# Kernel optimization log

Hardware: AMD Instinct MI355X
Metric: run time of the kernel (lower is better)

The kernel has to match this reference:

```python
import jax, jax.numpy as jnp
import numpy as np
from jax import lax

ANCHOR_LENGTHS = (1.0, 2.0, 3.0, 4.0, 5.0, 7.0, 9.0)
B, C, LF = 8, 512, 8192
A = len(ANCHOR_LENGTHS)
PRE_K, POST_K = 600, 100          # pre/post NMS topk (propose defaults)
SCORE_TH, IOU_TH = 0.1, 0.5


def setup_inputs() -> dict:
    key = jax.random.key(0)
    ks = jax.random.split(key, 7)
    def n(k, shape, scale=1.0):
        return jax.random.normal(k, shape, dtype=jnp.float32) * scale
    return {
        "feat": n(ks[0], (B, C, LF)),
        "conv_w": n(ks[1], (C, C, 3), 0.02),
        "conv_b": n(ks[2], (C,), 0.02),
        "obj_w": n(ks[3], (A, C), 0.02),
        "obj_b": n(ks[4], (A,), 0.02),
        "reg_w": n(ks[5], (2 * A, C), 0.02),
        "reg_b": n(ks[6], (2 * A,), 0.02),
    }


def make_anchors_1d(Lf):
    lengths = jnp.asarray(ANCHOR_LENGTHS, jnp.float32)  # [A]
    centers = jnp.arange(Lf, dtype=jnp.float32) + 0.5   # [Lf]
    start = centers[:, None] - 0.5 * lengths[None, :]
    end = centers[:, None] + 0.5 * lengths[None, :]
    return jnp.stack([start, end], axis=-1).reshape(Lf * A, 2)  # [Lf*A, 2]


def decode_deltas_to_boxes(anchors, deltas, Lf):
    # anchors [N,2], deltas [B,N,2]
    a_c = 0.5 * (anchors[:, 0] + anchors[:, 1])
    a_w = jnp.clip(anchors[:, 1] - anchors[:, 0], 1e-6)
    t_c = deltas[..., 0]
    t_w = jnp.clip(deltas[..., 1], -10.0, 10.0)
    c = a_c[None, :] + t_c * a_w[None, :]
    w = a_w[None, :] * jnp.exp(t_w)
    Lff = jnp.float32(Lf)
    start = jnp.clip(c - 0.5 * w, 0.0, Lff)
    end = jnp.clip(c + 0.5 * w, 0.0, Lff)
    eps = 1e-3
    end = jnp.minimum(jnp.maximum(end, start + eps), Lff)
    start = jnp.maximum(jnp.minimum(start, end - eps), 0.0)
    return jnp.stack([start, end], axis=-1)  # [B,N,2]


def _nms_keep(boxes, valid):
    # boxes [K,2] already sorted by descending score; valid [K] bool
    s, e = boxes[:, 0], boxes[:, 1]
    inter = jnp.clip(jnp.minimum(e[:, None], e[None, :]) -
                     jnp.maximum(s[:, None], s[None, :]), 0.0)
    w = e - s
    union = w[:, None] + w[None, :] - inter
    iou = inter / jnp.clip(union, 1e-6)  # [K,K]; matches torchvision 2D trick (y-extent 1)
    idx = jnp.arange(boxes.shape[0])
    def body(i, keep):
        sup = jnp.any(keep & (idx < i) & (iou[i] > IOU_TH))
        return keep.at[i].set(keep[i] & jnp.logical_not(sup))
    return lax.fori_loop(0, boxes.shape[0], body, valid)


def propose(obj_logits, boxes):
    # fixed-shape, batched version of RPN1D.propose (no fallback path):
    # outputs are padded to POST_K with a validity mask.
    scores = jax.nn.sigmoid(obj_logits)                    # [B,N]
    s_top, idx = lax.top_k(scores, PRE_K)                  # sorted desc
    bxs = jnp.take_along_axis(boxes, idx[:, :, None], axis=1)  # [B,K,2]
    valid = s_top >= SCORE_TH
    keep = jax.vmap(_nms_keep)(bxs, valid)                 # [B,K]
    s_kept = jnp.where(keep, s_top, -1.0)
    s_out, j = lax.top_k(s_kept, POST_K)                   # kept, in score order
    b_out = jnp.take_along_axis(bxs, j[:, :, None], axis=1)
    vmask = s_out > 0.0
    return (jnp.where(vmask[:, :, None], b_out, 0.0),
            jnp.where(vmask, s_out, 0.0),
            vmask)


def reference(feat, conv_w, conv_b, obj_w, obj_b, reg_w, reg_b):
    # feat [B,C,Lf]; conv1d k=3 pad=1 + relu
    h = lax.conv_general_dilated(feat, conv_w, window_strides=(1,),
                                 padding=((1, 1),),
                                 dimension_numbers=("NCH", "OIH", "NCH"))
    h = jax.nn.relu(h + conv_b[None, :, None])
    x = jnp.transpose(h, (0, 2, 1))                        # [B,Lf,C]
    obj = jnp.einsum("blc,ac->bla", x, obj_w) + obj_b      # [B,Lf,A]
    reg = jnp.einsum("blc,ac->bla", x, reg_w) + reg_b      # [B,Lf,2A]
    Bsz, Lf = x.shape[0], x.shape[1]
    obj = obj.reshape(Bsz, Lf * A)                          # [B,N]
    reg = reg.reshape(Bsz, Lf * A, 2)                       # [B,N,2]
    anchors = make_anchors_1d(Lf)                           # [N,2]
    boxes = decode_deltas_to_boxes(anchors, reg, Lf)        # [B,N,2]
    props, pscores, pmask = propose(obj, boxes)
    return obj, reg, anchors, props, pscores, pmask
```

## Files before the change

kernel.cpp:

```cpp
#include <hip/hip_runtime.h>

#define LF 8192
#define NB 8
#define NC 512
#define NA 7
#define NANCH 57344
#define PRE_K 600
#define POST_K 100

#define OBJ_OFF   0
#define REG_OFF   458752
#define ANCH_OFF  1376256
#define PROPS_OFF 1490944
#define PSC_OFF   1492544
#define PM_OFF    1493344

#define WF_BYTES   3145728
#define GHIST_OFF  WF_BYTES
#define GHIST_BYTES (8 * 65536 * 4)

typedef __attribute__((ext_vector_type(8))) short bf16x8;
typedef __attribute__((ext_vector_type(4))) float f32x4;

__device__ __forceinline__ unsigned short f2bf(float f) {
  unsigned u = __float_as_uint(f);
  u += 0x7fff + ((u >> 16) & 1);
  return (unsigned short)(u >> 16);
}
__device__ __forceinline__ float bf2f(unsigned short h) {
  return __uint_as_float(((unsigned)h) << 16);
}

__device__ __forceinline__ void cvt_split(float v0, float v1,
                                          unsigned& hw, unsigned& lw) {
  asm("v_cvt_pk_bf16_f32 %0, %1, %2" : "=v"(hw) : "v"(v0), "v"(v1));
  float h0f = __uint_as_float(hw << 16);
  float h1f = __uint_as_float(hw & 0xffff0000u);
  asm("v_cvt_pk_bf16_f32 %0, %1, %2" : "=v"(lw) : "v"(v0 - h0f), "v"(v1 - h1f));
}

__global__ void prep_w_k(const float* __restrict__ cw, unsigned short* __restrict__ wf,
                         float* __restrict__ out, unsigned* __restrict__ ghist) {
  int o = blockIdx.x * 256 + threadIdx.x;
  {
    size_t z = 2 * (size_t)o;
    if (z < ANCH_OFF) {
      out[z] = 0.f;
      if (z + 1 < ANCH_OFF) out[z + 1] = 0.f;
    }
  }
  if (o < 8 * 65536) ghist[o] = 0u;
  if (o < NANCH) {
    int l = o / 7, a = o - l * 7;
    float len = (float)(a + 1 + (a > 4 ? a - 4 : 0));
    float c = (float)l + 0.5f;
    out[ANCH_OFF + 2 * (size_t)o]     = c - 0.5f * len;
    out[ANCH_OFF + 2 * (size_t)o + 1] = c + 0.5f * len;
  }
  if (o >= 786432) return;
  int j    = o & 7;
  int lane = (o >> 3) & 63;
  int cotl = (o >> 9) & 7;
  int rem  = o >> 12;
  int tap  = rem % 3;
  int cc   = rem / 3;
  int co = (cc >> 4) * 128 + cotl * 16 + (lane & 15);
  int ci = (cc & 15) * 32 + (lane >> 4) * 8 + j;
  float w = cw[((size_t)co * 512 + ci) * 3 + tap];
  unsigned short hi = f2bf(w);
  unsigned short lo = f2bf(w - bf2f(hi));
  size_t base = ((((size_t)rem * 8 + cotl) * 2) * 64 + lane) * 8 + j;
  wf[base] = hi;
  wf[base + 512] = lo;
}

#define BUFSH 10400
__global__ __launch_bounds__(256) void conv_proj_k(
    const float* __restrict__ feat, const unsigned short* __restrict__ wfrag,
    const float* __restrict__ cbias, const float* __restrict__ obj_w,
    const float* __restrict__ obj_b, const float* __restrict__ reg_w,
    const float* __restrict__ reg_b, float* __restrict__ out)
{
  __shared__ __align__(16) char smem[41600];
  unsigned short* sb = (unsigned short*)smem;
  float* bufp = (float*)smem;

  const int tid  = threadIdx.x;
  const int l0   = blockIdx.x * 128;
  const int cob  = blockIdx.y;
  const int b    = blockIdx.z;
  const int lane = tid & 63, wave = tid >> 6;
  const int wm = wave >> 1, wn = wave & 1;
  const int quad = lane >> 4, l15 = lane & 15;

  const float* fb = feat + (size_t)b * 512 * LF;
  const bf16x8* wf8 = (const bf16x8*)wfrag;

  f32x4 acc[4][4];
  #pragma unroll
  for (int mt = 0; mt < 4; ++mt)
    #pragma unroll
    for (int nt = 0; nt < 4; ++nt) acc[mt][nt] = (f32x4){0.f, 0.f, 0.f, 0.f};

  const int r8 = tid & 7, cp2 = (tid >> 3) & 15, set = tid >> 7;

  const int brr = tid >> 4, bc2 = tid & 15;
  const int bl = (brr == 0) ? (l0 - 1) : (l0 + 128);
  const bool bok = (bl >= 0) && (bl < LF);

  float pv0[8], pv1[8], bv0 = 0.f, bv1 = 0.f;

  auto prefetch = [&](int ch) {
    const int cb = ch * 32;
    #pragma unroll
    for (int p = 0; p < 8; ++p) {
      int l = l0 + p * 16 + set * 8 + r8;
      pv0[p] = fb[(size_t)(cb + 2 * cp2) * LF + l];
      pv1[p] = fb[(size_t)(cb + 2 * cp2 + 1) * LF + l];
    }
    if (tid < 32 && bok) {
      bv0 = fb[(size_t)(cb + 2 * bc2) * LF + bl];
      bv1 = fb[(size_t)(cb + 2 * bc2 + 1) * LF + bl];
    }
  };
  auto stage = [&](int bi) {
    unsigned short* fh = sb + bi * BUFSH;
    unsigned short* fl = fh + 5200;
    #pragma unroll
    for (int p = 0; p < 8; ++p) {
      int row = p * 16 + set * 8 + r8;
      unsigned hw, lw;
      cvt_split(pv0[p], pv1[p], hw, lw);
      int e = (row + 1) * 40 + 2 * cp2;
      *(unsigned*)(fh + e) = hw;
      *(unsigned*)(fl + e) = lw;
    }
    if (tid < 32) {
      unsigned hw, lw;
      cvt_split(bv0, bv1, hw, lw);
      int e = (brr * 129) * 40 + 2 * bc2;
      *(unsigned*)(fh + e) = hw;
      *(unsigned*)(fl + e) = lw;
    }
  };

  prefetch(0);
  stage(0);
  prefetch(1);
  __syncthreads();

  for (int chunk = 0; chunk < 16; ++chunk) {
    const unsigned short* fh = sb + (chunk & 1) * BUFSH;
    const unsigned short* fl = fh + 5200;
    const int rem3 = (cob * 16 + chunk) * 3;

    bf16x8 AhA[4], AlA[4], AhB[4], AlB[4];
    bf16x8 Bh[4], Bl[4];

    auto loadA = [&](int tap, bf16x8* AH, bf16x8* AL) {
      #pragma unroll
      for (int mt = 0; mt < 4; ++mt) {
        int fi = (((rem3 + tap) * 8 + wm * 4 + mt) * 2) * 64 + lane;
        AH[mt] = wf8[fi];
        AL[mt] = wf8[fi + 64];
      }
    };
    auto loadB = [&](int tap) {
      #pragma unroll
      for (int nt = 0; nt < 4; ++nt) {
        int row = wn * 64 + nt * 16 + l15 + tap;
        int e = row * 40 + quad * 8;
        Bh[nt] = *(const bf16x8*)(fh + e);
        Bl[nt] = *(const bf16x8*)(fl + e);
      }
    };
    auto mfma_tap = [&](const bf16x8* AH, const bf16x8* AL) {
      __builtin_amdgcn_s_setprio(1);
      #pragma unroll
      for (int mt = 0; mt < 4; ++mt)
        #pragma unroll
        for (int nt = 0; nt < 4; ++nt) {
          acc[mt][nt] = __builtin_amdgcn_mfma_f32_16x16x32_bf16(AH[mt], Bh[nt], acc[mt][nt], 0, 0, 0);
          acc[mt][nt] = __builtin_amdgcn_mfma_f32_16x16x32_bf16(AH[mt], Bl[nt], acc[mt][nt], 0, 0, 0);
          acc[mt][nt] = __builtin_amdgcn_mfma_f32_16x16x32_bf16(AL[mt], Bh[nt], acc[mt][nt], 0, 0, 0);
        }
      __builtin_amdgcn_s_setprio(0);
    };

    loadA(0, AhA, AlA);
    if (chunk < 15) stage((chunk + 1) & 1);
    loadB(0);
    loadA(1, AhB, AlB);
    __builtin_amdgcn_sched_barrier(0);
    mfma_tap(AhA, AlA);
    loadB(1);
    loadA(2, AhA, AlA);
    __builtin_amdgcn_sched_barrier(0);
    mfma_tap(AhB, AlB);
    loadB(2);
    if (chunk < 14) prefetch(chunk + 2);
    mfma_tap(AhA, AlA);
    __syncthreads();
  }

  const int sg = tid >> 5;
  const int ll = tid & 31;
  int rc0 = 3 * sg     < 21 ? 3 * sg     : 20;
  int rc1 = 3 * sg + 1 < 21 ? 3 * sg + 1 : 20;
  int rc2 = 3 * sg + 2 < 21 ? 3 * sg + 2 : 20;
  const float* wr0 = (rc0 < 7) ? (obj_w + (size_t)rc0 * 512) : (reg_w + (size_t)(rc0 - 7) * 512);
  const float* wr1 = (rc1 < 7) ? (obj_w + (size_t)rc1 * 512) : (reg_w + (size_t)(rc1 - 7) * 512);
  const float* wr2 = (rc2 < 7) ? (obj_w + (size_t)rc2 * 512) : (reg_w + (size_t)(rc2 - 7) * 512);
  float pacc[3][4];
  #pragma unroll
  for (int q = 0; q < 3; ++q)
    #pragma unroll
    for (int m = 0; m < 4; ++m) pacc[q][m] = 0.f;

  #pragma unroll
  for (int h = 0; h < 2; ++h) {
    __syncthreads();
    if (wm == h) {
      #pragma unroll
      for (int mt = 0; mt < 4; ++mt) {
        f32x4 bv = *(const f32x4*)(cbias + cob * 128 + h * 64 + mt * 16 + quad * 4);
        #pragma unroll
        for (int nt = 0; nt < 4; ++nt) {
          int col = wn * 64 + nt * 16 + l15;
          #pragma unroll
          for (int r = 0; r < 4; ++r)
            bufp[(mt * 16 + quad * 4 + r) * 130 + col] = fmaxf(acc[mt][nt][r] + bv[r], 0.f);
        }
      }
    }
    __syncthreads();
    for (int c = 0; c < 64; ++c) {
      int cg = cob * 128 + h * 64 + c;
      float w0 = wr0[cg], w1 = wr1[cg], w2 = wr2[cg];
      #pragma unroll
      for (int m = 0; m < 4; ++m) {
        float hv = bufp[c * 130 + ll + 32 * m];
        pacc[0][m] = fmaf(w0, hv, pacc[0][m]);
        pacc[1][m] = fmaf(w1, hv, pacc[1][m]);
        pacc[2][m] = fmaf(w2, hv, pacc[2][m]);
      }
    }
  }

  const size_t ob = (size_t)b * NANCH;
  #pragma unroll
  for (int q = 0; q < 3; ++q) {
    int r = 3 * sg + q;
    if (r < 21) {
      #pragma unroll
      for (int m = 0; m < 4; ++m) {
        int l = l0 + ll + 32 * m;
        float v = pacc[q][m] + ((cob == 0) ? ((r < 7) ? obj_b[r] : reg_b[r - 7]) : 0.f);
        if (r < 7) atomicAdd(&out[OBJ_OFF + ob + (size_t)l * 7 + r], v);
        else { int rr = r - 7; atomicAdd(&out[REG_OFF + (ob + (size_t)l * 7 + (rr >> 1)) * 2 + (rr & 1)], v); }
      }
    }
  }
}

__device__ __forceinline__ unsigned keybits(float x) {
  unsigned u = __float_as_uint(x);
  return (u & 0x80000000u) ? ~u : (u | 0x80000000u);
}

__global__ __launch_bounds__(256) void hist_k(const float* __restrict__ out,
                                              unsigned* __restrict__ ghist) {
  const int b = blockIdx.y;
  const float* obj = out + OBJ_OFF + (size_t)b * NANCH;
  unsigned* h = ghist + (size_t)b * 65536;
  const int base = blockIdx.x * 256 + threadIdx.x;
  float v[8];
  #pragma unroll
  for (int k = 0; k < 8; ++k) v[k] = obj[base + k * 7168];
  #pragma unroll
  for (int k = 0; k < 8; ++k) {
    unsigned bin = keybits(v[k]) >> 16;
    unsigned phys = ((bin & 255u) << 8) | (bin >> 8);
    atomicAdd(&h[phys], 1u);
  }
}

__global__ __launch_bounds__(1024) void propose_k(float* __restrict__ out,
                                                  const unsigned* __restrict__ ghist) {
  const int b = blockIdx.x;
  const int tid = threadIdx.x;
  const int lane = tid & 63;
  const int wave = tid >> 6;

  __shared__ unsigned long long pool[PRE_K * 10];
  __shared__ unsigned part[1024];
  __shared__ unsigned coarse[256];
  __shared__ float bs[PRE_K], be[PRE_K], bsc[PRE_K];
  __shared__ unsigned long long vwords[10];
  __shared__ int scal[6];

  unsigned long long* keys = pool;
  const float* obj = out + OBJ_OFF + (size_t)b * NANCH;
  const unsigned* gh = ghist + (size_t)b * 65536;

  if (tid < 10) vwords[tid] = 0ull;
  if (tid == 0) scal[2] = 0;

  {
    const int q = tid >> 8, h8 = tid & 255;
    unsigned s = 0;
    #pragma unroll 8
    for (int lo = 0; lo < 64; ++lo) s += gh[((unsigned)(q * 64 + lo) << 8) | (unsigned)h8];
    part[tid] = s;
  }
  __syncthreads();
  if (tid < 256) coarse[tid] = part[tid] + part[tid + 256] + part[tid + 512] + part[tid + 768];
  __syncthreads();
  for (int off = 1; off < 256; off <<= 1) {
    unsigned v = 0, add = 0;
    if (tid < 256) { v = coarse[tid]; add = (tid + off < 256) ? coarse[tid + off] : 0u; }
    __syncthreads();
    if (tid < 256) coarse[tid] = v + add;
    __syncthreads();
  }
  if (tid < 256) {
    unsigned sfx  = coarse[tid];
    unsigned sfx1 = (tid < 255) ? coarse[tid + 1] : 0u;
    if (sfx >= (unsigned)PRE_K && sfx1 < (unsigned)PRE_K) { scal[0] = tid; scal[1] = (int)sfx1; }
  }
  __syncthreads();
  const int hi8 = scal[0];
  const int before1 = scal[1];
  __syncthreads();
  if (tid < 256) coarse[tid] = gh[((unsigned)tid << 8) | (unsigned)hi8];
  __syncthreads();
  for (int off = 1; off < 256; off <<= 1) {
    unsigned v = 0, add = 0;
    if (tid < 256) { v = coarse[tid]; add = (tid + off < 256) ? coarse[tid + off] : 0u; }
    __syncthreads();
    if (tid < 256) coarse[tid] = v + add;
    __syncthreads();
  }
  if (tid < 256) {
    unsigned sfx  = coarse[tid];
    unsigned sfx1 = (tid < 255) ? coarse[tid + 1] : 0u;
    if (before1 + (int)sfx >= PRE_K && before1 + (int)sfx1 < PRE_K) scal[4] = tid;
  }
  __syncthreads();
  const unsigned Tbits = ((((unsigned)hi8 << 8) | (unsigned)scal[4]) << 16);

  for (int it = 0; it < 7; ++it) {
    float v[8];
    #pragma unroll
    for (int k = 0; k < 8; ++k) v[k] = obj[it * 8192 + k * 1024 + tid];
    #pragma unroll
    for (int k = 0; k < 8; ++k) {
      unsigned u = keybits(v[k]);
      if (u >= Tbits) {
        int p = atomicAdd(&scal[2], 1);
        if (p < 1024)
          keys[p] = ((unsigned long long)u << 32) |
                    (unsigned long long)(~(unsigned)(it * 8192 + k * 1024 + tid));
      }
    }
  }
  __syncthreads();
  const int cnt = scal[2];
  if (tid >= cnt) keys[tid] = 0ull;
  for (unsigned k = 2; k <= 1024; k <<= 1) {
    for (unsigned j = k >> 1; j > 0; j >>= 1) {
      __syncthreads();
      unsigned idx = tid, partner = idx ^ j;
      if (partner > idx) {
        unsigned long long a = keys[idx], c = keys[partner];
        bool up = ((idx & k) == 0);
        if (up ? (a < c) : (a > c)) { keys[idx] = c; keys[partner] = a; }
      }
    }
  }
  __syncthreads();
  if (tid < PRE_K) {
    const int t = tid;
    unsigned long long kv = keys[t];
    unsigned u  = (unsigned)(kv >> 32);
    unsigned i2 = ~((unsigned)kv);
    unsigned ub = (u & 0x80000000u) ? (u & 0x7fffffffu) : ~u;
    float logit = __uint_as_float(ub);
    float score = 1.f / (1.f + expf(-logit));
    int li = (int)(i2 / 7u);
    int a  = (int)(i2 - (unsigned)li * 7u);
    float alen = (float)(a + 1 + (a > 4 ? a - 4 : 0));
    const float* rp = out + REG_OFF + ((size_t)b * NANCH + i2) * 2;
    float tc = rp[0];
    float tw = fminf(fmaxf(rp[1], -10.f), 10.f);
    float cc = (float)li + 0.5f + tc * alen;
    float ww = alen * expf(tw);
    float s0 = cc - 0.5f * ww;
    float e0 = cc + 0.5f * ww;
    s0 = fminf(fmaxf(s0, 0.f), (float)LF);
    e0 = fminf(fmaxf(e0, 0.f), (float)LF);
    e0 = fminf(fmaxf(e0, s0 + 1e-3f), (float)LF);
    s0 = fmaxf(fminf(s0, e0 - 1e-3f), 0.f);
    bs[t] = s0; be[t] = e0; bsc[t] = score;
    if (score >= 0.1f) atomicOr(&vwords[t >> 6], 1ull << (t & 63));
  }
  __syncthreads();
  for (int widx = tid; widx < PRE_K * 10; widx += 1024) {
    int j = widx / 10;
    int w = widx - j * 10;
    int base = w * 64;
    unsigned long long m = 0ull;
    if (base + 63 > j) {
      float sj = bs[j], ej = be[j];
      float wj = ej - sj;
      for (int bit = 0; bit < 64; ++bit) {
        int i3 = base + bit;
        if (i3 > j && i3 < PRE_K) {
          float inter = fmaxf(fminf(ej, be[i3]) - fmaxf(sj, bs[i3]), 0.f);
          float uni = wj + (be[i3] - bs[i3]) - inter;
          float iou = inter / fmaxf(uni, 1e-6f);
          if (iou > 0.5f) m |= (1ull << bit);
        }
      }
    }
    pool[widx] = m;
  }
  __syncthreads();
  if (wave == 0) {
    unsigned long long rem = 0ull;
    unsigned long long vw = (lane < 10) ? vwords[lane] : 0ull;
    unsigned long long mrow = (lane < 10) ? pool[lane] : 0ull;
    int kept = 0;
    for (int g = 0; g < PRE_K && kept < POST_K; g += 8) {
      unsigned long long n0 = (lane < 10 && g + 1 < PRE_K) ? pool[(g + 1) * 10 + lane] : 0ull;
      unsigned long long n1 = (lane < 10 && g + 2 < PRE_K) ? pool[(g + 2) * 10 + lane] : 0ull;
      unsigned long long n2 = (lane < 10 && g + 3 < PRE_K) ? pool[(g + 3) * 10 + lane] : 0ull;
      unsigned long long n3 = (lane < 10 && g + 4 < PRE_K) ? pool[(g + 4) * 10 + lane] : 0ull;
      unsigned long long n4 = (lane < 10 && g + 5 < PRE_K) ? pool[(g + 5) * 10 + lane] : 0ull;
      unsigned long long n5 = (lane < 10 && g + 6 < PRE_K) ? pool[(g + 6) * 10 + lane] : 0ull;
      unsigned long long n6 = (lane < 10 && g + 7 < PRE_K) ? pool[(g + 7) * 10 + lane] : 0ull;
      unsigned long long n7 = (lane < 10 && g + 8 < PRE_K) ? pool[(g + 8) * 10 + lane] : 0ull;
      #pragma unroll
      for (int k = 0; k < 8; ++k) {
        int i3 = g + k;
        if (i3 < PRE_K) {
          unsigned long long avail = vw & ~rem;
          unsigned long long ow = __shfl(avail, i3 >> 6);
          if (((ow >> (i3 & 63)) & 1ull) && kept < POST_K) {
            rem |= mrow;
            if (lane == 0) {
              out[PROPS_OFF + (size_t)b * 200 + 2 * kept]     = bs[i3];
              out[PROPS_OFF + (size_t)b * 200 + 2 * kept + 1] = be[i3];
              out[PSC_OFF + (size_t)b * 100 + kept] = bsc[i3];
              out[PM_OFF  + (size_t)b * 100 + kept] = 1.0f;
            }
            ++kept;
          }
        }
        mrow = (k == 0) ? n0 : (k == 1) ? n1 : (k == 2) ? n2 : (k == 3) ? n3
             : (k == 4) ? n4 : (k == 5) ? n5 : (k == 6) ? n6 : n7;
      }
    }
    if (lane == 0) scal[3] = kept;
  }
  __syncthreads();
  const int kf = scal[3];
  if (tid < POST_K && tid >= kf) {
    out[PROPS_OFF + (size_t)b * 200 + 2 * tid]     = 0.f;
    out[PROPS_OFF + (size_t)b * 200 + 2 * tid + 1] = 0.f;
    out[PSC_OFF + (size_t)b * 100 + tid] = 0.f;
    out[PM_OFF  + (size_t)b * 100 + tid] = 0.f;
  }
}

extern "C" void kernel_launch(void* const* d_in, const int* in_sizes, int n_in,
                              void* d_out, int out_size, void* d_ws, size_t ws_size,
                              hipStream_t stream) {
  const float* feat = (const float*)d_in[0];
  const float* cw   = (const float*)d_in[1];
  const float* cb   = (const float*)d_in[2];
  const float* ow   = (const float*)d_in[3];
  const float* obb  = (const float*)d_in[4];
  const float* rw   = (const float*)d_in[5];
  const float* rb   = (const float*)d_in[6];
  float* out = (float*)d_out;
  unsigned short* wf = (unsigned short*)d_ws;
  unsigned* ghist = (unsigned*)((char*)d_ws + GHIST_OFF);

  hipLaunchKernelGGL(prep_w_k, dim3(3072), dim3(256), 0, stream, cw, wf, out, ghist);
  hipLaunchKernelGGL(conv_proj_k, dim3(64, 4, 8), dim3(256), 0, stream,
                     feat, wf, cb, ow, obb, rw, rb, out);
  hipLaunchKernelGGL(hist_k, dim3(28, 8), dim3(256), 0, stream, out, ghist);
  hipLaunchKernelGGL(propose_k, dim3(8), dim3(1024), 0, stream, out, ghist);
}
```

Before: 606.2 us.

## Loop output-channel blocks inside conv block and fuse histogram into epilogue

Each conv block now iterates over all four 128-channel output blocks itself, so the projection partial sums stay in registers and are written with plain stores instead of float atomics. This removes the output zeroing in prep and the separate histogram kernel, since the objectness histogram is built in the conv epilogue. The trade-off is a grid cut to 512 blocks, down from 2048, so each block does four times the work and occupancy drops. Feature tiles are also re-read and re-converted from global memory once per channel block.

```diff
diff --git a/kernel.cpp b/kernel.cpp
--- a/kernel.cpp
+++ b/kernel.cpp
@@ -39,16 +39,14 @@
   asm("v_cvt_pk_bf16_f32 %0, %1, %2" : "=v"(lw) : "v"(v0 - h0f), "v"(v1 - h1f));
 }
 
+__device__ __forceinline__ unsigned keybits(float x) {
+  unsigned u = __float_as_uint(x);
+  return (u & 0x80000000u) ? ~u : (u | 0x80000000u);
+}
+
 __global__ void prep_w_k(const float* __restrict__ cw, unsigned short* __restrict__ wf,
                          float* __restrict__ out, unsigned* __restrict__ ghist) {
   int o = blockIdx.x * 256 + threadIdx.x;
-  {
-    size_t z = 2 * (size_t)o;
-    if (z < ANCH_OFF) {
-      out[z] = 0.f;
-      if (z + 1 < ANCH_OFF) out[z + 1] = 0.f;
-    }
-  }
   if (o < 8 * 65536) ghist[o] = 0u;
   if (o < NANCH) {
     int l = o / 7, a = o - l * 7;
@@ -79,7 +77,8 @@
     const float* __restrict__ feat, const unsigned short* __restrict__ wfrag,
     const float* __restrict__ cbias, const float* __restrict__ obj_w,
     const float* __restrict__ obj_b, const float* __restrict__ reg_w,
-    const float* __restrict__ reg_b, float* __restrict__ out)
+    const float* __restrict__ reg_b, float* __restrict__ out,
+    unsigned* __restrict__ ghist)
 {
   __shared__ __align__(16) char smem[41600];
   unsigned short* sb = (unsigned short*)smem;
@@ -87,7 +86,6 @@
 
   const int tid  = threadIdx.x;
   const int l0   = blockIdx.x * 128;
-  const int cob  = blockIdx.y;
   const int b    = blockIdx.z;
   const int lane = tid & 63, wave = tid >> 6;
   const int wm = wave >> 1, wn = wave & 1;
@@ -95,12 +93,6 @@
 
   const float* fb = feat + (size_t)b * 512 * LF;
   const bf16x8* wf8 = (const bf16x8*)wfrag;
-
-  f32x4 acc[4][4];
-  #pragma unroll
-  for (int mt = 0; mt < 4; ++mt)
-    #pragma unroll
-    for (int nt = 0; nt < 4; ++nt) acc[mt][nt] = (f32x4){0.f, 0.f, 0.f, 0.f};
 
   const int r8 = tid & 7, cp2 = (tid >> 3) & 15, set = tid >> 7;
 
@@ -143,65 +135,6 @@
       *(unsigned*)(fl + e) = lw;
     }
   };
-
-  prefetch(0);
-  stage(0);
-  prefetch(1);
-  __syncthreads();
-
-  for (int chunk = 0; chunk < 16; ++chunk) {
-    const unsigned short* fh = sb + (chunk & 1) * BUFSH;
-    const unsigned short* fl = fh + 5200;
-    const int rem3 = (cob * 16 + chunk) * 3;
-
-    bf16x8 AhA[4], AlA[4], AhB[4], AlB[4];
-    bf16x8 Bh[4], Bl[4];
-
-    auto loadA = [&](int tap, bf16x8* AH, bf16x8* AL) {
-      #pragma unroll
-      for (int mt = 0; mt < 4; ++mt) {
-        int fi = (((rem3 + tap) * 8 + wm * 4 + mt) * 2) * 64 + lane;
-        AH[mt] = wf8[fi];
-        AL[mt] = wf8[fi + 64];
-      }
-    };
-    auto loadB = [&](int tap) {
-      #pragma unroll
-      for (int nt = 0; nt < 4; ++nt) {
-        int row = wn * 64 + nt * 16 + l15 + tap;
-        int e = row * 40 + quad * 8;
-        Bh[nt] = *(const bf16x8*)(fh + e);
-        Bl[nt] = *(const bf16x8*)(fl + e);
-      }
-    };
-    auto mfma_tap = [&](const bf16x8* AH, const bf16x8* AL) {
-      __builtin_amdgcn_s_setprio(1);
-      #pragma unroll
-      for (int mt = 0; mt < 4; ++mt)
-        #pragma unroll
-        for (int nt = 0; nt < 4; ++nt) {
-          acc[mt][nt] = __builtin_amdgcn_mfma_f32_16x16x32_bf16(AH[mt], Bh[nt], acc[mt][nt], 0, 0, 0);
-          acc[mt][nt] = __builtin_amdgcn_mfma_f32_16x16x32_bf16(AH[mt], Bl[nt], acc[mt][nt], 0, 0, 0);
-          acc[mt][nt] = __builtin_amdgcn_mfma_f32_16x16x32_bf16(AL[mt], Bh[nt], acc[mt][nt], 0, 0, 0);
-        }
-      __builtin_amdgcn_s_setprio(0);
-    };
-
-    loadA(0, AhA, AlA);
-    if (chunk < 15) stage((chunk + 1) & 1);
-    loadB(0);
-    loadA(1, AhB, AlB);
-    __builtin_amdgcn_sched_barrier(0);
-    mfma_tap(AhA, AlA);
-    loadB(1);
-    loadA(2, AhA, AlA);
-    __builtin_amdgcn_sched_barrier(0);
-    mfma_tap(AhB, AlB);
-    loadB(2);
-    if (chunk < 14) prefetch(chunk + 2);
-    mfma_tap(AhA, AlA);
-    __syncthreads();
-  }
 
   const int sg = tid >> 5;
   const int ll = tid & 31;
@@ -217,37 +150,106 @@
     #pragma unroll
     for (int m = 0; m < 4; ++m) pacc[q][m] = 0.f;
 
-  #pragma unroll
-  for (int h = 0; h < 2; ++h) {
+  for (int cob = 0; cob < 4; ++cob) {
+    f32x4 acc[4][4];
+    #pragma unroll
+    for (int mt = 0; mt < 4; ++mt)
+      #pragma unroll
+      for (int nt = 0; nt < 4; ++nt) acc[mt][nt] = (f32x4){0.f, 0.f, 0.f, 0.f};
+
+    if (cob > 0) __syncthreads();
+    prefetch(0);
+    stage(0);
+    prefetch(1);
     __syncthreads();
-    if (wm == h) {
-      #pragma unroll
-      for (int mt = 0; mt < 4; ++mt) {
-        f32x4 bv = *(const f32x4*)(cbias + cob * 128 + h * 64 + mt * 16 + quad * 4);
+
+    for (int chunk = 0; chunk < 16; ++chunk) {
+      const unsigned short* fh = sb + (chunk & 1) * BUFSH;
+      const unsigned short* fl = fh + 5200;
+      const int rem3 = (cob * 16 + chunk) * 3;
+
+      bf16x8 AhA[4], AlA[4], AhB[4], AlB[4];
+      bf16x8 Bh[4], Bl[4];
+
+      auto loadA = [&](int tap, bf16x8* AH, bf16x8* AL) {
+        #pragma unroll
+        for (int mt = 0; mt < 4; ++mt) {
+          int fi = (((rem3 + tap) * 8 + wm * 4 + mt) * 2) * 64 + lane;
+          AH[mt] = wf8[fi];
+          AL[mt] = wf8[fi + 64];
+        }
+      };
+      auto loadB = [&](int tap) {
         #pragma unroll
         for (int nt = 0; nt < 4; ++nt) {
-          int col = wn * 64 + nt * 16 + l15;
+          int row = wn * 64 + nt * 16 + l15 + tap;
+          int e = row * 40 + quad * 8;
+          Bh[nt] = *(const bf16x8*)(fh + e);
+          Bl[nt] = *(const bf16x8*)(fl + e);
+        }
+      };
+      auto mfma_tap = [&](const bf16x8* AH, const bf16x8* AL) {
+        __builtin_amdgcn_s_setprio(1);
+        #pragma unroll
+        for (int mt = 0; mt < 4; ++mt)
           #pragma unroll
-          for (int r = 0; r < 4; ++r)
-            bufp[(mt * 16 + quad * 4 + r) * 130 + col] = fmaxf(acc[mt][nt][r] + bv[r], 0.f);
-        }
-      }
-    }
-    __syncthreads();
-    for (int c = 0; c < 64; ++c) {
-      int cg = cob * 128 + h * 64 + c;
-      float w0 = wr0[cg], w1 = wr1[cg], w2 = wr2[cg];
-      #pragma unroll
-      for (int m = 0; m < 4; ++m) {
-        float hv = bufp[c * 130 + ll + 32 * m];
-        pacc[0][m] = fmaf(w0, hv, pacc[0][m]);
-        pacc[1][m] = fmaf(w1, hv, pacc[1][m]);
-        pacc[2][m] = fmaf(w2, hv, pacc[2][m]);
+          for (int nt = 0; nt < 4; ++nt) {
+            acc[mt][nt] = __builtin_amdgcn_mfma_f32_16x16x32_bf16(AH[mt], Bh[nt], acc[mt][nt], 0, 0, 0);
+            acc[mt][nt] = __builtin_amdgcn_mfma_f32_16x16x32_bf16(AH[mt], Bl[nt], acc[mt][nt], 0, 0, 0);
+            acc[mt][nt] = __builtin_amdgcn_mfma_f32_16x16x32_bf16(AL[mt], Bh[nt], acc[mt][nt], 0, 0, 0);
+          }
+        __builtin_amdgcn_s_setprio(0);
+      };
+
+      loadA(0, AhA, AlA);
+      if (chunk < 15) stage((chunk + 1) & 1);
+      loadB(0);
+      loadA(1, AhB, AlB);
+      __builtin_amdgcn_sched_barrier(0);
+      mfma_tap(AhA, AlA);
+      loadB(1);
+      loadA(2, AhA, AlA);
+      __builtin_amdgcn_sched_barrier(0);
+      mfma_tap(AhB, AlB);
+      loadB(2);
+      if (chunk < 14) prefetch(chunk + 2);
+      mfma_tap(AhA, AlA);
+      __syncthreads();
+    }
+
+    #pragma unroll
+    for (int h = 0; h < 2; ++h) {
+      __syncthreads();
+      if (wm == h) {
+        #pragma unroll
+        for (int mt = 0; mt < 4; ++mt) {
+          f32x4 bv = *(const f32x4*)(cbias + cob * 128 + h * 64 + mt * 16 + quad * 4);
+          #pragma unroll
+          for (int nt = 0; nt < 4; ++nt) {
+            int col = wn * 64 + nt * 16 + l15;
+            #pragma unroll
+            for (int r = 0; r < 4; ++r)
+              bufp[(mt * 16 + quad * 4 + r) * 130 + col] = fmaxf(acc[mt][nt][r] + bv[r], 0.f);
+          }
+        }
+      }
+      __syncthreads();
+      for (int c = 0; c < 64; ++c) {
+        int cg = cob * 128 + h * 64 + c;
+        float w0 = wr0[cg], w1 = wr1[cg], w2 = wr2[cg];
+        #pragma unroll
+        for (int m = 0; m < 4; ++m) {
+          float hv = bufp[c * 130 + ll + 32 * m];
+          pacc[0][m] = fmaf(w0, hv, pacc[0][m]);
+          pacc[1][m] = fmaf(w1, hv, pacc[1][m]);
+          pacc[2][m] = fmaf(w2, hv, pacc[2][m]);
+        }
       }
     }
   }
 
   const size_t ob = (size_t)b * NANCH;
+  unsigned* gh = ghist + (size_t)b * 65536;
   #pragma unroll
   for (int q = 0; q < 3; ++q) {
     int r = 3 * sg + q;
@@ -255,33 +257,18 @@
       #pragma unroll
       for (int m = 0; m < 4; ++m) {
         int l = l0 + ll + 32 * m;
-        float v = pacc[q][m] + ((cob == 0) ? ((r < 7) ? obj_b[r] : reg_b[r - 7]) : 0.f);
-        if (r < 7) atomicAdd(&out[OBJ_OFF + ob + (size_t)l * 7 + r], v);
-        else { int rr = r - 7; atomicAdd(&out[REG_OFF + (ob + (size_t)l * 7 + (rr >> 1)) * 2 + (rr & 1)], v); }
-      }
-    }
-  }
-}
-
-__device__ __forceinline__ unsigned keybits(float x) {
-  unsigned u = __float_as_uint(x);
-  return (u & 0x80000000u) ? ~u : (u | 0x80000000u);
-}
-
-__global__ __launch_bounds__(256) void hist_k(const float* __restrict__ out,
-                                              unsigned* __restrict__ ghist) {
-  const int b = blockIdx.y;
-  const float* obj = out + OBJ_OFF + (size_t)b * NANCH;
-  unsigned* h = ghist + (size_t)b * 65536;
-  const int base = blockIdx.x * 256 + threadIdx.x;
-  float v[8];
-  #pragma unroll
-  for (int k = 0; k < 8; ++k) v[k] = obj[base + k * 7168];
-  #pragma unroll
-  for (int k = 0; k < 8; ++k) {
-    unsigned bin = keybits(v[k]) >> 16;
-    unsigned phys = ((bin & 255u) << 8) | (bin >> 8);
-    atomicAdd(&h[phys], 1u);
+        float v = pacc[q][m] + ((r < 7) ? obj_b[r] : reg_b[r - 7]);
+        if (r < 7) {
+          out[OBJ_OFF + ob + (size_t)l * 7 + r] = v;
+          unsigned bin = keybits(v) >> 16;
+          unsigned phys = ((bin & 255u) << 8) | (bin >> 8);
+          atomicAdd(&gh[phys], 1u);
+        } else {
+          int rr = r - 7;
+          out[REG_OFF + (ob + (size_t)l * 7 + (rr >> 1)) * 2 + (rr & 1)] = v;
+        }
+      }
+    }
   }
 }
 
@@ -488,8 +475,7 @@
   unsigned* ghist = (unsigned*)((char*)d_ws + GHIST_OFF);
 
   hipLaunchKernelGGL(prep_w_k, dim3(3072), dim3(256), 0, stream, cw, wf, out, ghist);
-  hipLaunchKernelGGL(conv_proj_k, dim3(64, 4, 8), dim3(256), 0, stream,
-                     feat, wf, cb, ow, obb, rw, rb, out);
-  hipLaunchKernelGGL(hist_k, dim3(28, 8), dim3(256), 0, stream, out, ghist);
+  hipLaunchKernelGGL(conv_proj_k, dim3(64, 1, 8), dim3(256), 0, stream,
+                     feat, wf, cb, ow, obb, rw, rb, out, ghist);
   hipLaunchKernelGGL(propose_k, dim3(8), dim3(1024), 0, stream, out, ghist);
 }
```

Measured after the change: 645.4 us. 1.06x slower.
